# Kernel tuning notes

Hardware: AMD Instinct MI355X
Metric: run time of the kernel (lower is better)

## Reference

```python
import jax, jax.numpy as jnp
import numpy as np

EPS = 1e-5

def _fake_quant(w, axis):
    # symmetric int8 fake-quant with straight-through estimator
    s = jnp.max(jnp.abs(w), axis=axis, keepdims=True) / 127.0 + 1e-8
    q = jnp.clip(jnp.round(w / s), -127.0, 127.0) * s
    return w + jax.lax.stop_gradient(q - w)

def _qconv1x1(x, w, b):
    # x: [B, C_in, Q, H, W]; w: [C_out, C_in] (1x1 kernel); weight fake-quantized
    wq = _fake_quant(w, axis=1)
    return jnp.einsum('bcqhw,oc->boqhw', x, wq) + b[None, :, None, None, None]

def setup_inputs() -> dict:
    key = jax.random.key(0)
    ks = jax.random.split(key, 12)
    B, C, Q, H, W = 8, 256, 4, 40, 40
    x = jax.random.normal(ks[0], (B, C, Q, H, W), dtype=jnp.float32)
    scale = 1.0 / np.sqrt(C)
    Wq = jax.random.normal(ks[1], (C, C), dtype=jnp.float32) * scale
    Wk = jax.random.normal(ks[2], (C, C), dtype=jnp.float32) * scale
    Wv = jax.random.normal(ks[3], (C, C), dtype=jnp.float32) * scale
    Wp = jax.random.normal(ks[4], (C, C), dtype=jnp.float32) * scale
    bq = jnp.zeros((C,), jnp.float32)
    bk = jnp.zeros((C,), jnp.float32)
    bv = jnp.zeros((C,), jnp.float32)
    bp = jnp.zeros((C,), jnp.float32)
    gamma = jnp.ones((C,), jnp.float32)
    beta = jnp.zeros((C,), jnp.float32)
    return {"x": x, "Wq": Wq, "bq": bq, "Wk": Wk, "bk": bk,
            "Wv": Wv, "bv": bv, "Wp": Wp, "bp": bp,
            "gamma": gamma, "beta": beta}

def reference(x, Wq, bq, Wk, bk, Wv, bv, Wp, bp, gamma, beta):
    B, C, Q, H, W = x.shape
    q = _qconv1x1(x, Wq, bq)
    k = _qconv1x1(x, Wk, bk)
    v = _qconv1x1(x, Wv, bv)
    # per-rotation channel attention: [B, Q=4, C, H*W]
    qh = q.reshape(B, C, Q, H * W).transpose(0, 2, 1, 3)
    kh = k.reshape(B, C, Q, H * W).transpose(0, 2, 1, 3)
    vh = v.reshape(B, C, Q, H * W).transpose(0, 2, 1, 3)
    scale = 1.0 / jnp.sqrt(jnp.float32(C // 4))
    attn = jnp.einsum('bqcn,bqdn->bqcd', qh, kh) * scale  # [B,4,C,C]
    attn = jax.nn.softmax(attn, axis=-1)
    out = jnp.einsum('bqcd,bqdn->bqcn', attn, vh)  # [B,4,C,HW]
    out = out.transpose(0, 2, 1, 3).reshape(B, C, Q, H, W)
    out = _qconv1x1(out, Wp, bp)
    # IQBN: per-channel batchnorm with int8 fake-quantized gamma
    mean = jnp.mean(out, axis=(0, 2, 3, 4), keepdims=True)
    var = jnp.var(out, axis=(0, 2, 3, 4), keepdims=True)
    g = _fake_quant(gamma, axis=None)[None, :, None, None, None]
    b = beta[None, :, None, None, None]
    out = (out - mean) * jax.lax.rsqrt(var + EPS) * g + b
    return out
```

## Files before the change

kernel.cpp:

```cpp
#include <hip/hip_runtime.h>
#include <math.h>

#define BB 8
#define CCH 256
#define QQ 4
#define NN 1600
#define BQN 32
#define SP 51200
#define EPSF 1e-5f

typedef __attribute__((ext_vector_type(8))) short bf16x8;
typedef __attribute__((ext_vector_type(4))) float f32x4;

static __device__ inline ushort f2bf(float f) {
  union { float f; unsigned u; } v; v.f = f;
  return (ushort)((v.u + 0x7fffu + ((v.u >> 16) & 1u)) >> 16);
}
static __device__ inline float bf2f(ushort u) {
  union { unsigned u; float f; } v; v.u = ((unsigned)u) << 16;
  return v.f;
}
static __device__ inline void gld16(const ushort* g, ushort* l) {
  __builtin_amdgcn_global_load_lds(
      (const __attribute__((address_space(1))) unsigned int*)g,
      (__attribute__((address_space(3))) unsigned int*)l, 16, 0, 0);
}

__global__ __launch_bounds__(256)
void qp_kernel(const float* __restrict__ Wq, const float* __restrict__ Wk,
               const float* __restrict__ Wv, const float* __restrict__ Wp,
               const float* __restrict__ gamma, const float* __restrict__ x,
               ushort* __restrict__ wq, ushort* __restrict__ wk,
               ushort* __restrict__ wvT, ushort* __restrict__ wp,
               ushort* __restrict__ wqT, ushort* __restrict__ wkT,
               ushort* __restrict__ wpT, float* __restrict__ gq,
               ushort* __restrict__ xb, ushort* __restrict__ xT,
               float* __restrict__ rpart) {
  __shared__ float red[256];
  __shared__ ushort lT[64 * 66];
  int blk = blockIdx.x;
  int tid = threadIdx.x;
  if (blk < 1024) {
    int mat = blk >> 8;
    int row = blk & 255;
    const float* W = (mat == 0) ? Wq : (mat == 1) ? Wk : (mat == 2) ? Wv : Wp;
    float w = W[row * 256 + tid];
    red[tid] = fabsf(w);
    __syncthreads();
    for (int s = 128; s > 0; s >>= 1) {
      if (tid < s) red[tid] = fmaxf(red[tid], red[tid + s]);
      __syncthreads();
    }
    float s = red[0] / 127.0f + 1e-8f;
    float q = fminf(fmaxf(rintf(w / s), -127.0f), 127.0f) * s;
    ushort qb = f2bf(q);
    if (mat == 0)      { wq[row * 256 + tid] = qb; wqT[tid * 256 + row] = qb; }
    else if (mat == 1) { wk[row * 256 + tid] = qb; wkT[tid * 256 + row] = qb; }
    else if (mat == 2) { wvT[tid * 256 + row] = qb; }
    else               { wp[row * 256 + tid] = qb; wpT[tid * 256 + row] = qb; }
    return;
  }
  if (blk == 1024) {
    float g = gamma[tid];
    red[tid] = fabsf(g);
    __syncthreads();
    for (int s = 128; s > 0; s >>= 1) {
      if (tid < s) red[tid] = fmaxf(red[tid], red[tid + s]);
      __syncthreads();
    }
    float s = red[0] / 127.0f + 1e-8f;
    gq[tid] = fminf(fmaxf(rintf(g / s), -127.0f), 127.0f) * s;
    return;
  }
  int p = blk - 1025;
  int sx = p % 25;
  int rem = p / 25;
  int cy = rem & 3, bqi = rem >> 2;
  int b = bqi >> 2, q = bqi & 3;
  int s0 = sx * 64, c0 = cy * 64;
  int c = tid >> 2, nch = (tid & 3) * 16;
  const float* xp = x + ((size_t)(b * CCH + c0 + c) * QQ + q) * NN + s0 + nch;
  union { ushort u[16]; int4 v[2]; } nb;
  float s = 0.f;
#pragma unroll
  for (int j = 0; j < 4; j++) {
    float4 f = ((const float4*)xp)[j];
    ushort b0 = f2bf(f.x), b1 = f2bf(f.y), b2 = f2bf(f.z), b3 = f2bf(f.w);
    s += bf2f(b0) + bf2f(b1) + bf2f(b2) + bf2f(b3);
    nb.u[j * 4 + 0] = b0;
    nb.u[j * 4 + 1] = b1;
    nb.u[j * 4 + 2] = b2;
    nb.u[j * 4 + 3] = b3;
    lT[c * 66 + nch + j * 4 + 0] = b0;
    lT[c * 66 + nch + j * 4 + 1] = b1;
    lT[c * 66 + nch + j * 4 + 2] = b2;
    lT[c * 66 + nch + j * 4 + 3] = b3;
  }
  ushort* xbp = xb + (size_t)bqi * (CCH * NN) + (size_t)(c0 + c) * NN + s0 + nch;
  *(int4*)xbp = nb.v[0];
  *((int4*)xbp + 1) = nb.v[1];
  s += __shfl_down(s, 2);
  s += __shfl_down(s, 1);
  if ((tid & 3) == 0) rpart[((size_t)bqi * 25 + sx) * 256 + c0 + c] = s;
  __syncthreads();
  int n = tid >> 2, cch = (tid & 3) * 16;
  union { ushort u[16]; int4 v[2]; } o;
#pragma unroll
  for (int i = 0; i < 16; i++) o.u[i] = lT[(cch + i) * 66 + n];
  ushort* dst = xT + (size_t)(bqi * NN + s0 + n) * CCH + c0 + cch;
  *(int4*)dst = o.v[0];
  *((int4*)dst + 1) = o.v[1];
}

__global__ __launch_bounds__(256)
void gram_uv_kernel(const ushort* __restrict__ xb, ushort* __restrict__ Gh,
                    ushort* __restrict__ Gl,
                    const ushort* __restrict__ wqT, const ushort* __restrict__ wkT,
                    const float* __restrict__ rpart, float* __restrict__ r,
                    float* __restrict__ u, float* __restrict__ vv) {
  __shared__ __align__(16) char smem[16384];
  __shared__ float rs[256];
  int t = blockIdx.x, z = blockIdx.y;
  int tid = threadIdx.x;
  if (t == 10) {
    float rv = 0.f;
#pragma unroll
    for (int k = 0; k < 25; k++) rv += rpart[((size_t)z * 25 + k) * 256 + tid];
    rs[tid] = rv;
    r[z * 256 + tid] = rv;
    __syncthreads();
    float su = 0.f, sv = 0.f;
    for (int i = 0; i < 256; i++) {
      float rr = rs[i];
      su += bf2f(wqT[i * 256 + tid]) * rr;
      sv += bf2f(wkT[i * 256 + tid]) * rr;
    }
    u[z * 256 + tid] = su;
    vv[z * 256 + tid] = sv;
    return;
  }
  int ty = (t >= 4) + (t >= 7) + (t >= 9);
  int base = ty * 4 - (ty * (ty - 1)) / 2;
  int tx = ty + (t - base);
  int mBase = ty * 64, nBase = tx * 64;
  bool offd = (tx != ty);
  int wave = tid >> 6, lane = tid & 63;
  int wm = wave >> 1, wn = wave & 1;
  int col = lane & 15, quad = lane >> 4;
  const ushort* X = xb + (size_t)z * (CCH * NN);
  const ushort* gA = X + (size_t)(mBase + (tid >> 2)) * NN + (tid & 3) * 8;
  const ushort* gB = X + (size_t)(nBase + (tid >> 2)) * NN + (tid & 3) * 8;
  f32x4 acc[2][2];
#pragma unroll
  for (int i = 0; i < 2; i++)
#pragma unroll
    for (int j = 0; j < 2; j++) acc[i][j] = (f32x4){0.f, 0.f, 0.f, 0.f};

  const int nIter = NN / 32;
  gld16(gA, (ushort*)smem + tid * 8);
  gld16(gB, (ushort*)(smem + 4096) + tid * 8);
  for (int it = 0; it < nIter; ++it) {
    int cur = it & 1;
    __syncthreads();
    if (it + 1 < nIter) {
      int kt = (it + 1) << 5;
      char* bb = smem + (cur ^ 1) * 8192;
      gld16(gA + kt, (ushort*)bb + tid * 8);
      gld16(gB + kt, (ushort*)(bb + 4096) + tid * 8);
    }
    const ushort* lA = (const ushort*)(smem + cur * 8192);
    const ushort* lB = lA + 2048;
    bf16x8 af[2], bfr[2];
#pragma unroll
    for (int i = 0; i < 2; i++)
      af[i] = *(const bf16x8*)&lA[(wm * 32 + i * 16 + col) * 32 + quad * 8];
#pragma unroll
    for (int j = 0; j < 2; j++)
      bfr[j] = *(const bf16x8*)&lB[(wn * 32 + j * 16 + col) * 32 + quad * 8];
#pragma unroll
    for (int i = 0; i < 2; i++)
#pragma unroll
      for (int j = 0; j < 2; j++)
        acc[i][j] = __builtin_amdgcn_mfma_f32_16x16x32_bf16(af[i], bfr[j], acc[i][j], 0, 0, 0);
  }
  __syncthreads();
  float* lCw = (float*)smem + wave * 576;
#pragma unroll
  for (int i = 0; i < 2; i++) {
#pragma unroll
    for (int j = 0; j < 2; j++)
#pragma unroll
      for (int rg = 0; rg < 4; rg++)
        lCw[(quad * 4 + rg) * 36 + j * 16 + col] = acc[i][j][rg];
    int mrow0 = mBase + wm * 32 + i * 16;
    int nW = nBase + wn * 32;
    int rr = lane >> 2, cc = (lane & 3) * 8;
    union { ushort u[8]; int4 v; } oh, ol;
#pragma unroll
    for (int t8 = 0; t8 < 8; t8++) {
      float vfl = lCw[rr * 36 + cc + t8];
      ushort hh = f2bf(vfl);
      oh.u[t8] = hh;
      ol.u[t8] = f2bf(vfl - bf2f(hh));
    }
    size_t off = (size_t)z * 65536 + (size_t)(mrow0 + rr) * 256 + nW + cc;
    *(int4*)(Gh + off) = oh.v;
    *(int4*)(Gl + off) = ol.v;
    if (offd) {
      int nn = lane >> 1, mh = (lane & 1) * 8;
      union { ushort u[8]; int4 v; } th, tl;
#pragma unroll
      for (int t8 = 0; t8 < 8; t8++) {
        float vfl = lCw[(mh + t8) * 36 + nn];
        ushort hh = f2bf(vfl);
        th.u[t8] = hh;
        tl.u[t8] = f2bf(vfl - bf2f(hh));
      }
      size_t offT = (size_t)z * 65536 + (size_t)(nW + nn) * 256 + mrow0 + mh;
      *(int4*)(Gh + offT) = th.v;
      *(int4*)(Gl + offT) = tl.v;
    }
  }
}

__global__ __launch_bounds__(256)
void spk_kernel(const ushort* __restrict__ wq, const ushort* __restrict__ Gh,
                const ushort* __restrict__ Gl, const ushort* __restrict__ wk,
                const float* __restrict__ ug, const float* __restrict__ vg,
                const float* __restrict__ bqv, const float* __restrict__ bkv,
                const float* __restrict__ bvv,
                ushort* __restrict__ P, float* __restrict__ pb) {
  __shared__ __align__(16) char smem[103424];
  int z = blockIdx.y, mBase = blockIdx.x * 32;
  int tid = threadIdx.x, wave = tid >> 6, lane = tid & 63;
  int col = lane & 15, quad = lane >> 4;
  int rA = tid >> 2, sub = (tid & 3) * 8;
  const ushort* Ghz = Gh + (size_t)z * 65536;
  const ushort* Glz = Gl + (size_t)z * 65536;
  ushort* M1h_l = (ushort*)(smem + 69632);
  ushort* M1l_l = M1h_l + 8448;

  f32x4 acc[2][4];
#pragma unroll
  for (int i = 0; i < 2; i++)
#pragma unroll
    for (int j = 0; j < 4; j++) acc[i][j] = (f32x4){0.f, 0.f, 0.f, 0.f};

  auto s1_load = [&](int buf, int kt) {
    ushort* L = (ushort*)(smem + buf * 34816);
    if (tid < 128)
      gld16(wq + (size_t)(mBase + rA) * 256 + kt + sub, L + tid * 8);
    ushort* Lh = L + 1024;
    ushort* Ll = L + 9216;
#pragma unroll
    for (int q = 0; q < 4; q++) {
      int n = q * 64 + rA;
      gld16(Ghz + (size_t)n * 256 + kt + sub, Lh + (q * 256 + tid) * 8);
      gld16(Glz + (size_t)n * 256 + kt + sub, Ll + (q * 256 + tid) * 8);
    }
  };
  s1_load(0, 0);
  for (int it = 0; it < 8; ++it) {
    int cur = it & 1;
    __syncthreads();
    if (it + 1 < 8) s1_load(cur ^ 1, (it + 1) * 32);
    const ushort* L = (const ushort*)(smem + cur * 34816);
    const ushort* lA = L;
    const ushort* lBh = L + 1024;
    const ushort* lBl = L + 9216;
    bf16x8 af[2], bh[4], bl[4];
#pragma unroll
    for (int i = 0; i < 2; i++)
      af[i] = *(const bf16x8*)&lA[(i * 16 + col) * 32 + quad * 8];
#pragma unroll
    for (int j = 0; j < 4; j++) {
      bh[j] = *(const bf16x8*)&lBh[(wave * 64 + j * 16 + col) * 32 + quad * 8];
      bl[j] = *(const bf16x8*)&lBl[(wave * 64 + j * 16 + col) * 32 + quad * 8];
    }
#pragma unroll
    for (int i = 0; i < 2; i++)
#pragma unroll
      for (int j = 0; j < 4; j++) {
        acc[i][j] = __builtin_amdgcn_mfma_f32_16x16x32_bf16(af[i], bh[j], acc[i][j], 0, 0, 0);
        acc[i][j] = __builtin_amdgcn_mfma_f32_16x16x32_bf16(af[i], bl[j], acc[i][j], 0, 0, 0);
      }
  }
#pragma unroll
  for (int i = 0; i < 2; i++)
#pragma unroll
    for (int j = 0; j < 4; j++)
#pragma unroll
      for (int rg = 0; rg < 4; rg++) {
        int ml = i * 16 + quad * 4 + rg;
        int cg = wave * 64 + j * 16 + col;
        float vfl = acc[i][j][rg];
        ushort hh = f2bf(vfl);
        M1h_l[ml * 264 + cg] = hh;
        M1l_l[ml * 264 + cg] = f2bf(vfl - bf2f(hh));
      }

  f32x4 acc2[2][4];
#pragma unroll
  for (int i = 0; i < 2; i++)
#pragma unroll
    for (int j = 0; j < 4; j++) acc2[i][j] = (f32x4){0.f, 0.f, 0.f, 0.f};
  auto s2_load = [&](int buf, int kt) {
    ushort* L = (ushort*)(smem + buf * 34816);
#pragma unroll
    for (int q = 0; q < 4; q++)
      gld16(wk + (size_t)(q * 64 + rA) * 256 + kt + sub, L + (q * 256 + tid) * 8);
  };
  s2_load(0, 0);
  for (int it = 0; it < 8; ++it) {
    int cur = it & 1;
    __syncthreads();
    if (it + 1 < 8) s2_load(cur ^ 1, (it + 1) * 32);
    const ushort* lB = (const ushort*)(smem + cur * 34816);
    int kt = it * 32;
    bf16x8 ah[2], al[2], bfr[4];
#pragma unroll
    for (int i = 0; i < 2; i++) {
      ah[i] = *(const bf16x8*)&M1h_l[(i * 16 + col) * 264 + kt + quad * 8];
      al[i] = *(const bf16x8*)&M1l_l[(i * 16 + col) * 264 + kt + quad * 8];
    }
#pragma unroll
    for (int j = 0; j < 4; j++)
      bfr[j] = *(const bf16x8*)&lB[(wave * 64 + j * 16 + col) * 32 + quad * 8];
#pragma unroll
    for (int i = 0; i < 2; i++)
#pragma unroll
      for (int j = 0; j < 4; j++) {
        acc2[i][j] = __builtin_amdgcn_mfma_f32_16x16x32_bf16(ah[i], bfr[j], acc2[i][j], 0, 0, 0);
        acc2[i][j] = __builtin_amdgcn_mfma_f32_16x16x32_bf16(al[i], bfr[j], acc2[i][j], 0, 0, 0);
      }
  }
  __syncthreads();

  float* Sb = (float*)(smem + 69632);
  float bkc[4], vvc[4];
#pragma unroll
  for (int j = 0; j < 4; j++) {
    int cg = wave * 64 + j * 16 + col;
    bkc[j] = bkv[cg];
    vvc[j] = vg[z * 256 + cg];
  }
#pragma unroll
  for (int i = 0; i < 2; i++)
#pragma unroll
    for (int rg = 0; rg < 4; rg++) {
      int ml = i * 16 + quad * 4 + rg;
      int rglob = mBase + ml;
      float uu = ug[z * 256 + rglob];
      float bqc = bqv[rglob];
#pragma unroll
      for (int j = 0; j < 4; j++)
        Sb[ml * 260 + wave * 64 + j * 16 + col] =
            0.125f * (acc2[i][j][rg] + uu * bkc[j] + bqc * vvc[j] + 1600.0f * bqc * bkc[j]);
    }
  __syncthreads();

  float4 bv4 = *(const float4*)(bvv + lane * 4);
#pragma unroll
  for (int rr8 = 0; rr8 < 8; ++rr8) {
    int rloc = wave * 8 + rr8;
    f32x4 sv = *(const f32x4*)&Sb[rloc * 260 + lane * 4];
    float x0 = sv[0], x1 = sv[1], x2 = sv[2], x3 = sv[3];
    float m = fmaxf(fmaxf(x0, x1), fmaxf(x2, x3));
#pragma unroll
    for (int s = 32; s > 0; s >>= 1) m = fmaxf(m, __shfl_xor(m, s));
    float e0 = expf(x0 - m), e1 = expf(x1 - m), e2 = expf(x2 - m), e3 = expf(x3 - m);
    float t = e0 + e1 + e2 + e3;
#pragma unroll
    for (int s = 32; s > 0; s >>= 1) t += __shfl_xor(t, s);
    float is = 1.0f / t;
    float p0 = e0 * is, p1 = e1 * is, p2 = e2 * is, p3 = e3 * is;
    union { ushort u[4]; uint2 v; } o;
    o.u[0] = f2bf(p0); o.u[1] = f2bf(p1); o.u[2] = f2bf(p2); o.u[3] = f2bf(p3);
    *(uint2*)(P + (size_t)z * 65536 + (size_t)(mBase + rloc) * 256 + lane * 4) = o.v;
    float d = p0 * bv4.x + p1 * bv4.y + p2 * bv4.z + p3 * bv4.w;
#pragma unroll
    for (int s = 32; s > 0; s >>= 1) d += __shfl_xor(d, s);
    if (lane == 0) pb[z * 256 + mBase + rloc] = d;
  }
}

__global__ __launch_bounds__(256)
void pt_kernel(const ushort* __restrict__ P, const ushort* __restrict__ wvT,
               const ushort* __restrict__ wp,
               ushort* __restrict__ Tm, ushort* __restrict__ TmT,
               float* __restrict__ m_acc, float* __restrict__ v_acc) {
  __shared__ __align__(16) char smem[53760];
  int z = blockIdx.y, cs = blockIdx.x * 32;
  int tid = threadIdx.x, wave = tid >> 6, lane = tid & 63;
  int col = lane & 15, quad = lane >> 4;
  int rA = tid >> 2, sub = (tid & 3) * 8;
  if (blockIdx.x == 0 && blockIdx.y == 0) {
    m_acc[tid] = 0.f;
    v_acc[tid] = 0.f;
  }
  const ushort* Pz = P + (size_t)z * 65536;
  ushort* N1b = (ushort*)(smem + 36864);

  f32x4 acc[4][2];
#pragma unroll
  for (int i = 0; i < 4; i++)
#pragma unroll
    for (int j = 0; j < 2; j++) acc[i][j] = (f32x4){0.f, 0.f, 0.f, 0.f};
  auto s3_load = [&](int buf, int kt) {
    ushort* L = (ushort*)(smem + buf * 18432);
#pragma unroll
    for (int q = 0; q < 4; q++)
      gld16(Pz + (size_t)(q * 64 + rA) * 256 + kt + sub, L + (q * 256 + tid) * 8);
    if (tid < 128)
      gld16(wvT + (size_t)(cs + rA) * 256 + kt + sub, L + 8192 + tid * 8);
  };
  s3_load(0, 0);
  for (int it = 0; it < 8; ++it) {
    int cur = it & 1;
    __syncthreads();
    if (it + 1 < 8) s3_load(cur ^ 1, (it + 1) * 32);
    const ushort* lP = (const ushort*)(smem + cur * 18432);
    const ushort* lV = lP + 8192;
    bf16x8 af[4], bfr[2];
#pragma unroll
    for (int i = 0; i < 4; i++)
      af[i] = *(const bf16x8*)&lP[(wave * 64 + i * 16 + col) * 32 + quad * 8];
#pragma unroll
    for (int j = 0; j < 2; j++)
      bfr[j] = *(const bf16x8*)&lV[(j * 16 + col) * 32 + quad * 8];
#pragma unroll
    for (int i = 0; i < 4; i++)
#pragma unroll
      for (int j = 0; j < 2; j++)
        acc[i][j] = __builtin_amdgcn_mfma_f32_16x16x32_bf16(af[i], bfr[j], acc[i][j], 0, 0, 0);
  }
#pragma unroll
  for (int i = 0; i < 4; i++)
#pragma unroll
    for (int j = 0; j < 2; j++)
#pragma unroll
      for (int rg = 0; rg < 4; rg++) {
        int e = wave * 64 + i * 16 + quad * 4 + rg;
        int cl = j * 16 + col;
        N1b[cl * 264 + e] = f2bf(acc[i][j][rg]);
      }

  f32x4 acc2[4][2];
#pragma unroll
  for (int i = 0; i < 4; i++)
#pragma unroll
    for (int j = 0; j < 2; j++) acc2[i][j] = (f32x4){0.f, 0.f, 0.f, 0.f};
  auto s4_load = [&](int buf, int kt) {
    ushort* L = (ushort*)(smem + buf * 18432);
#pragma unroll
    for (int q = 0; q < 4; q++)
      gld16(wp + (size_t)(q * 64 + rA) * 256 + kt + sub, L + (q * 256 + tid) * 8);
  };
  s4_load(0, 0);
  for (int it = 0; it < 8; ++it) {
    int cur = it & 1;
    __syncthreads();
    if (it + 1 < 8) s4_load(cur ^ 1, (it + 1) * 32);
    const ushort* lW = (const ushort*)(smem + cur * 18432);
    int kt = it * 32;
    bf16x8 af[4], bfr[2];
#pragma unroll
    for (int i = 0; i < 4; i++)
      af[i] = *(const bf16x8*)&lW[(wave * 64 + i * 16 + col) * 32 + quad * 8];
#pragma unroll
    for (int j = 0; j < 2; j++)
      bfr[j] = *(const bf16x8*)&N1b[(j * 16 + col) * 264 + kt + quad * 8];
#pragma unroll
    for (int i = 0; i < 4; i++)
#pragma unroll
      for (int j = 0; j < 2; j++)
        acc2[i][j] = __builtin_amdgcn_mfma_f32_16x16x32_bf16(af[i], bfr[j], acc2[i][j], 0, 0, 0);
  }
  __syncthreads();
  float* lCw = (float*)smem + wave * 576;
#pragma unroll
  for (int i = 0; i < 4; i++) {
#pragma unroll
    for (int j = 0; j < 2; j++)
#pragma unroll
      for (int rg = 0; rg < 4; rg++)
        lCw[(quad * 4 + rg) * 36 + j * 16 + col] = acc2[i][j][rg];
    int oW = wave * 64 + i * 16;
    int rr = lane >> 2, cc = (lane & 3) * 8;
    union { ushort u[8]; int4 v; } o;
#pragma unroll
    for (int t8 = 0; t8 < 8; t8++) o.u[t8] = f2bf(lCw[rr * 36 + cc + t8]);
    *(int4*)(Tm + (size_t)z * 65536 + (size_t)(oW + rr) * 256 + cs + cc) = o.v;
    int nn = lane >> 1, mh = (lane & 1) * 8;
    union { ushort u[8]; int4 v; } o2;
#pragma unroll
    for (int t8 = 0; t8 < 8; t8++) o2.u[t8] = f2bf(lCw[(mh + t8) * 36 + nn]);
    *(int4*)(TmT + (size_t)z * 65536 + (size_t)(cs + nn) * 256 + oW + mh) = o2.v;
  }
}

__global__ __launch_bounds__(256)
void dsq_bo_kernel(const ushort* __restrict__ Tm, const ushort* __restrict__ Gh,
                   const ushort* __restrict__ Gl,
                   const ushort* __restrict__ wpT, const ushort* __restrict__ TmT,
                   const float* __restrict__ pb, const float* __restrict__ rb,
                   const float* __restrict__ bp, float* __restrict__ bo,
                   float* __restrict__ m_acc, float* __restrict__ v_acc) {
  __shared__ __align__(16) char smem[24576];
  int blk = blockIdx.x;
  int tid = threadIdx.x;
  if (blk >= 512) {
    int z = blk - 512;
    float* sp = (float*)smem;
    float* sr = sp + 256;
    sp[tid] = pb[z * 256 + tid];
    sr[tid] = rb[z * 256 + tid];
    __syncthreads();
    float bv = bp[tid], d1 = 0.f;
    const ushort* Tz = TmT + (size_t)z * 65536;
    for (int c = 0; c < 256; c++) {
      bv += bf2f(wpT[c * 256 + tid]) * sp[c];
      d1 += bf2f(Tz[c * 256 + tid]) * sr[c];
    }
    bo[z * 256 + tid] = bv;
    atomicAdd(m_acc + tid, d1 + 1600.0f * bv);
    atomicAdd(v_acc + tid, 2.0f * bv * d1 + 1600.0f * bv * bv);
    return;
  }
  int z = blk >> 4;
  int mBase = ((blk >> 2) & 3) * 64, nBase = (blk & 3) * 64;
  int wave = tid >> 6, lane = tid & 63;
  int wm = wave >> 1, wn = wave & 1;
  int col = lane & 15, quad = lane >> 4;
  int srow = tid >> 2, skc = (tid & 3) * 8;
  const ushort* Tz = Tm + (size_t)z * 65536;
  const ushort* gA = Tz + (size_t)(mBase + srow) * 256 + skc;
  const ushort* gB = Gh + (size_t)z * 65536 + (size_t)(nBase + srow) * 256 + skc;
  const ushort* gX = Gl + (size_t)z * 65536 + (size_t)(nBase + srow) * 256 + skc;

  f32x4 acc[2][2];
#pragma unroll
  for (int i = 0; i < 2; i++)
#pragma unroll
    for (int j = 0; j < 2; j++) acc[i][j] = (f32x4){0.f, 0.f, 0.f, 0.f};

  {
    char* bb = smem;
    gld16(gA, (ushort*)bb + tid * 8);
    gld16(gB, (ushort*)(bb + 4096) + tid * 8);
    gld16(gX, (ushort*)(bb + 8192) + tid * 8);
  }
  for (int it = 0; it < 8; ++it) {
    int cur = it & 1;
    __syncthreads();
    if (it + 1 < 8) {
      int kt = (it + 1) * 32;
      char* bb = smem + (cur ^ 1) * 12288;
      gld16(gA + kt, (ushort*)bb + tid * 8);
      gld16(gB + kt, (ushort*)(bb + 4096) + tid * 8);
      gld16(gX + kt, (ushort*)(bb + 8192) + tid * 8);
    }
    const ushort* lA = (const ushort*)(smem + cur * 12288);
    const ushort* lB = lA + 2048;
    const ushort* lX = lA + 4096;
    bf16x8 af[2], bfv[2], xf[2];
#pragma unroll
    for (int i = 0; i < 2; i++)
      af[i] = *(const bf16x8*)&lA[(wm * 32 + i * 16 + col) * 32 + quad * 8];
#pragma unroll
    for (int j = 0; j < 2; j++) {
      bfv[j] = *(const bf16x8*)&lB[(wn * 32 + j * 16 + col) * 32 + quad * 8];
      xf[j]  = *(const bf16x8*)&lX[(wn * 32 + j * 16 + col) * 32 + quad * 8];
    }
#pragma unroll
    for (int i = 0; i < 2; i++)
#pragma unroll
      for (int j = 0; j < 2; j++) {
        acc[i][j] = __builtin_amdgcn_mfma_f32_16x16x32_bf16(af[i], bfv[j], acc[i][j], 0, 0, 0);
        acc[i][j] = __builtin_amdgcn_mfma_f32_16x16x32_bf16(af[i], xf[j], acc[i][j], 0, 0, 0);
      }
  }
#pragma unroll
  for (int i = 0; i < 2; i++) {
    int mr = mBase + wm * 32 + i * 16 + quad * 4;
#pragma unroll
    for (int rg = 0; rg < 4; rg++) {
      float p = 0.f;
#pragma unroll
      for (int j = 0; j < 2; j++)
        p += acc[i][j][rg] * bf2f(Tz[(mr + rg) * 256 + nBase + wn * 32 + j * 16 + col]);
      p += __shfl_down(p, 8);
      p += __shfl_down(p, 4);
      p += __shfl_down(p, 2);
      p += __shfl_down(p, 1);
      if (col == 0) atomicAdd(v_acc + mr + rg, p);
    }
  }
}

__global__ __launch_bounds__(256)
void final_kernel(const ushort* __restrict__ Tm, const ushort* __restrict__ xT,
                  const float* __restrict__ bo, const float* __restrict__ m_acc,
                  const float* __restrict__ v_acc, const float* __restrict__ gq,
                  const float* __restrict__ beta, float* __restrict__ out) {
  __shared__ __align__(16) char smem[32768];
  float* lC = (float*)smem;
  int z = blockIdx.z;
  int mBase = blockIdx.y * 128, nBase = blockIdx.x * 128;
  int tid = threadIdx.x, wave = tid >> 6, lane = tid & 63;
  int wm = wave >> 1, wn = wave & 1;
  int col = lane & 15, quad = lane >> 4;
  int srow = tid >> 2, skc = (tid & 3) * 8;
  const ushort* Az = Tm + (size_t)z * 65536;
  const ushort* Bz = xT + (size_t)z * (NN * 256);
  const ushort* gA  = Az + (size_t)(mBase + srow) * 256 + skc;
  const ushort* gA2 = gA + 64 * 256;
  int br1 = nBase + srow;      br1 = br1 < NN ? br1 : NN - 1;
  int br2 = nBase + 64 + srow; br2 = br2 < NN ? br2 : NN - 1;
  const ushort* gB  = Bz + (size_t)br1 * 256 + skc;
  const ushort* gB2 = Bz + (size_t)br2 * 256 + skc;
  ushort* sA1[2]; ushort* sA2[2]; ushort* sB1[2]; ushort* sB2[2];
#pragma unroll
  for (int b = 0; b < 2; b++) {
    ushort* lAb = (ushort*)(smem + b * 16384);
    ushort* lBb = (ushort*)(smem + b * 16384 + 8192);
    sA1[b] = &lAb[srow * 32 + skc];
    sA2[b] = &lAb[(64 + srow) * 32 + skc];
    sB1[b] = &lBb[srow * 32 + skc];
    sB2[b] = &lBb[(64 + srow) * 32 + skc];
  }
  f32x4 acc[4][4];
#pragma unroll
  for (int i = 0; i < 4; i++)
#pragma unroll
    for (int j = 0; j < 4; j++) acc[i][j] = (f32x4){0.f, 0.f, 0.f, 0.f};

  const int nIter = 8;
  gld16(gA, sA1[0]); gld16(gA2, sA2[0]); gld16(gB, sB1[0]); gld16(gB2, sB2[0]);
  for (int it = 0; it < nIter; ++it) {
    int cur = it & 1;
    __syncthreads();
    if (it + 1 < nIter) {
      int kt = (it + 1) << 5, nxt = cur ^ 1;
      gld16(gA + kt, sA1[nxt]); gld16(gA2 + kt, sA2[nxt]);
      gld16(gB + kt, sB1[nxt]); gld16(gB2 + kt, sB2[nxt]);
    }
    const ushort* lAc = (const ushort*)(smem + cur * 16384);
    const ushort* lBc = (const ushort*)(smem + cur * 16384 + 8192);
    bf16x8 af[4], bfr[4];
#pragma unroll
    for (int i = 0; i < 4; i++)
      af[i] = *(const bf16x8*)&lAc[(wm * 64 + i * 16 + col) * 32 + quad * 8];
#pragma unroll
    for (int j = 0; j < 4; j++)
      bfr[j] = *(const bf16x8*)&lBc[(wn * 64 + j * 16 + col) * 32 + quad * 8];
#pragma unroll
    for (int i = 0; i < 4; i++)
#pragma unroll
      for (int j = 0; j < 4; j++)
        acc[i][j] = __builtin_amdgcn_mfma_f32_16x16x32_bf16(af[i], bfr[j], acc[i][j], 0, 0, 0);
  }
  __syncthreads();
  float* lCw = lC + wave * 16 * 68;
  int mW = mBase + wm * 64, nW = nBase + wn * 64;
  int b = z >> 2, q = z & 3;
  const float inv = 1.0f / (float)SP;
#pragma unroll
  for (int i = 0; i < 4; i++) {
#pragma unroll
    for (int j = 0; j < 4; j++)
#pragma unroll
      for (int rg = 0; rg < 4; rg++)
        lCw[(quad * 4 + rg) * 68 + j * 16 + col] = acc[i][j][rg];
    int mrow0 = mW + i * 16;
    int rr = lane & 15, cc = lane >> 4;
    int n0 = nW + cc * 16;
    int o = mrow0 + rr;
    float bi = bo[(size_t)z * 256 + o];
    float mean = m_acc[o] * inv;
    float var = v_acc[o] * inv - mean * mean;
    float scl = rsqrtf(var + EPSF) * gq[o];
    float be = beta[o];
    if (n0 < NN) {
      float* C = out + (size_t)b * (CCH * QQ * NN)
               + (size_t)o * (QQ * NN) + (size_t)q * NN + n0;
#pragma unroll
      for (int v = 0; v < 4; v++) {
        float4 f;
        f.x = (lCw[rr * 68 + cc * 16 + v * 4 + 0] + bi - mean) * scl + be;
        f.y = (lCw[rr * 68 + cc * 16 + v * 4 + 1] + bi - mean) * scl + be;
        f.z = (lCw[rr * 68 + cc * 16 + v * 4 + 2] + bi - mean) * scl + be;
        f.w = (lCw[rr * 68 + cc * 16 + v * 4 + 3] + bi - mean) * scl + be;
        *(float4*)(C + v * 4) = f;
      }
    }
  }
}

extern "C" void kernel_launch(void* const* d_in, const int* in_sizes, int n_in,
                              void* d_out, int out_size, void* d_ws, size_t ws_size,
                              hipStream_t stream) {
  const float* x     = (const float*)d_in[0];
  const float* Wq    = (const float*)d_in[1];
  const float* bq    = (const float*)d_in[2];
  const float* Wk    = (const float*)d_in[3];
  const float* bk    = (const float*)d_in[4];
  const float* Wv    = (const float*)d_in[5];
  const float* bv    = (const float*)d_in[6];
  const float* Wp    = (const float*)d_in[7];
  const float* bp    = (const float*)d_in[8];
  const float* gamma = (const float*)d_in[9];
  const float* beta  = (const float*)d_in[10];
  float* out = (float*)d_out;

  ushort* h    = (ushort*)d_ws;
  ushort* wq   = h;
  ushort* wk   = wq + 65536;
  ushort* wp   = wk + 65536;
  ushort* wvT  = wp + 65536;
  ushort* wqT  = wvT + 65536;
  ushort* wkT  = wqT + 65536;
  ushort* wpT  = wkT + 65536;
  ushort* xb   = wpT + 65536;
  ushort* xT   = xb + (size_t)BQN * CCH * NN;
  ushort* Gh   = xT + (size_t)BQN * CCH * NN;
  ushort* Gl   = Gh + (size_t)BQN * 65536;
  ushort* P    = Gl + (size_t)BQN * 65536;
  ushort* Tm   = P + (size_t)BQN * 65536;
  ushort* TmT  = Tm + (size_t)BQN * 65536;
  float*  r    = (float*)(TmT + (size_t)BQN * 65536);
  float*  u    = r + 8192;
  float*  vv   = u + 8192;
  float*  pb   = vv + 8192;
  float*  bo   = pb + 8192;
  float*  m_acc = bo + 8192;
  float*  v_acc = m_acc + 256;
  float*  gq   = v_acc + 256;
  float*  rpart = gq + 256;

  qp_kernel<<<4225, 256, 0, stream>>>(Wq, Wk, Wv, Wp, gamma, x,
                                      wq, wk, wvT, wp, wqT, wkT, wpT, gq,
                                      xb, xT, rpart);
  gram_uv_kernel<<<dim3(11, BQN), 256, 0, stream>>>(xb, Gh, Gl, wqT, wkT,
                                                    rpart, r, u, vv);
  spk_kernel<<<dim3(8, BQN), 256, 0, stream>>>(wq, Gh, Gl, wk, u, vv, bq, bk, bv, P, pb);
  pt_kernel<<<dim3(8, BQN), 256, 0, stream>>>(P, wvT, wp, Tm, TmT, m_acc, v_acc);
  dsq_bo_kernel<<<544, 256, 0, stream>>>(Tm, Gh, Gl, wpT, TmT, pb, r, bp,
                                         bo, m_acc, v_acc);
  final_kernel<<<dim3(13, 2, BQN), 256, 0, stream>>>(Tm, xT, bo, m_acc, v_acc,
                                                     gq, beta, out);
}
```

Baseline: 254.6 us.

## Halve row tiles in spk/pt kernels and read operands directly from global memory

The spk and pt kernels now handle 16-row/column tiles instead of 32, which doubles the grid to 512 blocks. They also drop the LDS double-buffered global_load_lds staging and load MFMA operands straight from global memory (L2-cached) into registers. A block-index swizzle spreads consecutive blocks across batch slices. Shared memory per block shrinks sharply, which should raise occupancy and spread the work over more CUs. The cost is redundant global/L2 traffic, since each weight tile is reread by more blocks with no LDS reuse, and the loads are no longer overlapped through explicit prefetch.

```diff
diff --git a/kernel.cpp b/kernel.cpp
--- a/kernel.cpp
+++ b/kernel.cpp
@@ -19,6 +19,9 @@
 static __device__ inline float bf2f(ushort u) {
   union { unsigned u; float f; } v; v.u = ((unsigned)u) << 16;
   return v.f;
+}
+static __device__ inline bf16x8 ldg8(const ushort* p) {
+  return *(const bf16x8*)p;
 }
 static __device__ inline void gld16(const ushort* g, ushort* l) {
   __builtin_amdgcn_global_load_lds(
@@ -230,139 +233,91 @@
                 const float* __restrict__ bqv, const float* __restrict__ bkv,
                 const float* __restrict__ bvv,
                 ushort* __restrict__ P, float* __restrict__ pb) {
-  __shared__ __align__(16) char smem[103424];
-  int z = blockIdx.y, mBase = blockIdx.x * 32;
-  int tid = threadIdx.x, wave = tid >> 6, lane = tid & 63;
+  __shared__ __align__(16) char smem[16896];
+  ushort* M1h_l = (ushort*)smem;
+  ushort* M1l_l = M1h_l + 4224;
+  int lin = blockIdx.x + 16 * blockIdx.y;
+  int nl = (lin & 7) * 64 + (lin >> 3);
+  int mBase = (nl & 15) * 16, z = nl >> 4;
+  int tid = threadIdx.x, w = tid >> 6, lane = tid & 63;
   int col = lane & 15, quad = lane >> 4;
-  int rA = tid >> 2, sub = (tid & 3) * 8;
   const ushort* Ghz = Gh + (size_t)z * 65536;
   const ushort* Glz = Gl + (size_t)z * 65536;
-  ushort* M1h_l = (ushort*)(smem + 69632);
-  ushort* M1l_l = M1h_l + 8448;
-
-  f32x4 acc[2][4];
-#pragma unroll
-  for (int i = 0; i < 2; i++)
-#pragma unroll
-    for (int j = 0; j < 4; j++) acc[i][j] = (f32x4){0.f, 0.f, 0.f, 0.f};
-
-  auto s1_load = [&](int buf, int kt) {
-    ushort* L = (ushort*)(smem + buf * 34816);
-    if (tid < 128)
-      gld16(wq + (size_t)(mBase + rA) * 256 + kt + sub, L + tid * 8);
-    ushort* Lh = L + 1024;
-    ushort* Ll = L + 9216;
-#pragma unroll
-    for (int q = 0; q < 4; q++) {
-      int n = q * 64 + rA;
-      gld16(Ghz + (size_t)n * 256 + kt + sub, Lh + (q * 256 + tid) * 8);
-      gld16(Glz + (size_t)n * 256 + kt + sub, Ll + (q * 256 + tid) * 8);
-    }
-  };
-  s1_load(0, 0);
-  for (int it = 0; it < 8; ++it) {
-    int cur = it & 1;
-    __syncthreads();
-    if (it + 1 < 8) s1_load(cur ^ 1, (it + 1) * 32);
-    const ushort* L = (const ushort*)(smem + cur * 34816);
-    const ushort* lA = L;
-    const ushort* lBh = L + 1024;
-    const ushort* lBl = L + 9216;
-    bf16x8 af[2], bh[4], bl[4];
-#pragma unroll
-    for (int i = 0; i < 2; i++)
-      af[i] = *(const bf16x8*)&lA[(i * 16 + col) * 32 + quad * 8];
+
+  f32x4 acc[4];
+#pragma unroll
+  for (int j = 0; j < 4; j++) acc[j] = (f32x4){0.f, 0.f, 0.f, 0.f};
+  bf16x8 af[8];
+  {
+    const ushort* pA = wq + (size_t)(mBase + col) * 256 + quad * 8;
+#pragma unroll
+    for (int kk = 0; kk < 8; kk++) af[kk] = ldg8(pA + kk * 32);
+  }
+#pragma unroll
+  for (int kk = 0; kk < 8; kk++) {
 #pragma unroll
     for (int j = 0; j < 4; j++) {
-      bh[j] = *(const bf16x8*)&lBh[(wave * 64 + j * 16 + col) * 32 + quad * 8];
-      bl[j] = *(const bf16x8*)&lBl[(wave * 64 + j * 16 + col) * 32 + quad * 8];
-    }
-#pragma unroll
-    for (int i = 0; i < 2; i++)
-#pragma unroll
-      for (int j = 0; j < 4; j++) {
-        acc[i][j] = __builtin_amdgcn_mfma_f32_16x16x32_bf16(af[i], bh[j], acc[i][j], 0, 0, 0);
-        acc[i][j] = __builtin_amdgcn_mfma_f32_16x16x32_bf16(af[i], bl[j], acc[i][j], 0, 0, 0);
-      }
-  }
-#pragma unroll
-  for (int i = 0; i < 2; i++)
-#pragma unroll
-    for (int j = 0; j < 4; j++)
-#pragma unroll
-      for (int rg = 0; rg < 4; rg++) {
-        int ml = i * 16 + quad * 4 + rg;
-        int cg = wave * 64 + j * 16 + col;
-        float vfl = acc[i][j][rg];
-        ushort hh = f2bf(vfl);
-        M1h_l[ml * 264 + cg] = hh;
-        M1l_l[ml * 264 + cg] = f2bf(vfl - bf2f(hh));
-      }
-
-  f32x4 acc2[2][4];
-#pragma unroll
-  for (int i = 0; i < 2; i++)
-#pragma unroll
-    for (int j = 0; j < 4; j++) acc2[i][j] = (f32x4){0.f, 0.f, 0.f, 0.f};
-  auto s2_load = [&](int buf, int kt) {
-    ushort* L = (ushort*)(smem + buf * 34816);
-#pragma unroll
-    for (int q = 0; q < 4; q++)
-      gld16(wk + (size_t)(q * 64 + rA) * 256 + kt + sub, L + (q * 256 + tid) * 8);
-  };
-  s2_load(0, 0);
-  for (int it = 0; it < 8; ++it) {
-    int cur = it & 1;
-    __syncthreads();
-    if (it + 1 < 8) s2_load(cur ^ 1, (it + 1) * 32);
-    const ushort* lB = (const ushort*)(smem + cur * 34816);
-    int kt = it * 32;
-    bf16x8 ah[2], al[2], bfr[4];
-#pragma unroll
-    for (int i = 0; i < 2; i++) {
-      ah[i] = *(const bf16x8*)&M1h_l[(i * 16 + col) * 264 + kt + quad * 8];
-      al[i] = *(const bf16x8*)&M1l_l[(i * 16 + col) * 264 + kt + quad * 8];
-    }
-#pragma unroll
-    for (int j = 0; j < 4; j++)
-      bfr[j] = *(const bf16x8*)&lB[(wave * 64 + j * 16 + col) * 32 + quad * 8];
-#pragma unroll
-    for (int i = 0; i < 2; i++)
-#pragma unroll
-      for (int j = 0; j < 4; j++) {
-        acc2[i][j] = __builtin_amdgcn_mfma_f32_16x16x32_bf16(ah[i], bfr[j], acc2[i][j], 0, 0, 0);
-        acc2[i][j] = __builtin_amdgcn_mfma_f32_16x16x32_bf16(al[i], bfr[j], acc2[i][j], 0, 0, 0);
-      }
-  }
+      size_t ro = (size_t)(w * 64 + j * 16 + col) * 256 + kk * 32 + quad * 8;
+      bf16x8 bh = ldg8(Ghz + ro);
+      bf16x8 bl = ldg8(Glz + ro);
+      acc[j] = __builtin_amdgcn_mfma_f32_16x16x32_bf16(af[kk], bh, acc[j], 0, 0, 0);
+      acc[j] = __builtin_amdgcn_mfma_f32_16x16x32_bf16(af[kk], bl, acc[j], 0, 0, 0);
+    }
+  }
+#pragma unroll
+  for (int j = 0; j < 4; j++)
+#pragma unroll
+    for (int rg = 0; rg < 4; rg++) {
+      int ml = quad * 4 + rg;
+      int cg = w * 64 + j * 16 + col;
+      float vfl = acc[j][rg];
+      ushort hh = f2bf(vfl);
+      M1h_l[ml * 264 + cg] = hh;
+      M1l_l[ml * 264 + cg] = f2bf(vfl - bf2f(hh));
+    }
   __syncthreads();
 
-  float* Sb = (float*)(smem + 69632);
+  f32x4 acc2[4];
+#pragma unroll
+  for (int j = 0; j < 4; j++) acc2[j] = (f32x4){0.f, 0.f, 0.f, 0.f};
+#pragma unroll
+  for (int kk = 0; kk < 8; kk++) {
+    bf16x8 ah = *(const bf16x8*)&M1h_l[col * 264 + kk * 32 + quad * 8];
+    bf16x8 al = *(const bf16x8*)&M1l_l[col * 264 + kk * 32 + quad * 8];
+#pragma unroll
+    for (int j = 0; j < 4; j++) {
+      bf16x8 b = ldg8(wk + (size_t)(w * 64 + j * 16 + col) * 256 + kk * 32 + quad * 8);
+      acc2[j] = __builtin_amdgcn_mfma_f32_16x16x32_bf16(ah, b, acc2[j], 0, 0, 0);
+      acc2[j] = __builtin_amdgcn_mfma_f32_16x16x32_bf16(al, b, acc2[j], 0, 0, 0);
+    }
+  }
+  __syncthreads();
+
+  float* Sb = (float*)smem;
   float bkc[4], vvc[4];
 #pragma unroll
   for (int j = 0; j < 4; j++) {
-    int cg = wave * 64 + j * 16 + col;
+    int cg = w * 64 + j * 16 + col;
     bkc[j] = bkv[cg];
     vvc[j] = vg[z * 256 + cg];
   }
 #pragma unroll
-  for (int i = 0; i < 2; i++)
-#pragma unroll
-    for (int rg = 0; rg < 4; rg++) {
-      int ml = i * 16 + quad * 4 + rg;
-      int rglob = mBase + ml;
-      float uu = ug[z * 256 + rglob];
-      float bqc = bqv[rglob];
-#pragma unroll
-      for (int j = 0; j < 4; j++)
-        Sb[ml * 260 + wave * 64 + j * 16 + col] =
-            0.125f * (acc2[i][j][rg] + uu * bkc[j] + bqc * vvc[j] + 1600.0f * bqc * bkc[j]);
-    }
+  for (int rg = 0; rg < 4; rg++) {
+    int ml = quad * 4 + rg;
+    int rglob = mBase + ml;
+    float uu = ug[z * 256 + rglob];
+    float bqc = bqv[rglob];
+#pragma unroll
+    for (int j = 0; j < 4; j++)
+      Sb[ml * 260 + w * 64 + j * 16 + col] =
+          0.125f * (acc2[j][rg] + uu * bkc[j] + bqc * vvc[j] + 1600.0f * bqc * bkc[j]);
+  }
   __syncthreads();
 
   float4 bv4 = *(const float4*)(bvv + lane * 4);
 #pragma unroll
-  for (int rr8 = 0; rr8 < 8; ++rr8) {
-    int rloc = wave * 8 + rr8;
+  for (int rr4 = 0; rr4 < 4; ++rr4) {
+    int rloc = w * 4 + rr4;
     f32x4 sv = *(const f32x4*)&Sb[rloc * 260 + lane * 4];
     float x0 = sv[0], x1 = sv[1], x2 = sv[2], x3 = sv[3];
     float m = fmaxf(fmaxf(x0, x1), fmaxf(x2, x3));
@@ -389,113 +344,78 @@
                const ushort* __restrict__ wp,
                ushort* __restrict__ Tm, ushort* __restrict__ TmT,
                float* __restrict__ m_acc, float* __restrict__ v_acc) {
-  __shared__ __align__(16) char smem[53760];
-  int z = blockIdx.y, cs = blockIdx.x * 32;
-  int tid = threadIdx.x, wave = tid >> 6, lane = tid & 63;
+  __shared__ __align__(16) char smem[17664];
+  ushort* N1b = (ushort*)smem;
+  float* lCwB = (float*)(smem + 8448);
+  int lin = blockIdx.x + 16 * blockIdx.y;
+  int nl = (lin & 7) * 64 + (lin >> 3);
+  int cs = (nl & 15) * 16, z = nl >> 4;
+  int tid = threadIdx.x, w = tid >> 6, lane = tid & 63;
   int col = lane & 15, quad = lane >> 4;
-  int rA = tid >> 2, sub = (tid & 3) * 8;
-  if (blockIdx.x == 0 && blockIdx.y == 0) {
+  if (nl == 0) {
     m_acc[tid] = 0.f;
     v_acc[tid] = 0.f;
   }
   const ushort* Pz = P + (size_t)z * 65536;
-  ushort* N1b = (ushort*)(smem + 36864);
-
-  f32x4 acc[4][2];
+
+  f32x4 acc[4];
+#pragma unroll
+  for (int i = 0; i < 4; i++) acc[i] = (f32x4){0.f, 0.f, 0.f, 0.f};
+  bf16x8 bv8[8];
+  {
+    const ushort* pV = wvT + (size_t)(cs + col) * 256 + quad * 8;
+#pragma unroll
+    for (int kk = 0; kk < 8; kk++) bv8[kk] = ldg8(pV + kk * 32);
+  }
+#pragma unroll
+  for (int kk = 0; kk < 8; kk++) {
+#pragma unroll
+    for (int i = 0; i < 4; i++) {
+      bf16x8 a = ldg8(Pz + (size_t)(w * 64 + i * 16 + col) * 256 + kk * 32 + quad * 8);
+      acc[i] = __builtin_amdgcn_mfma_f32_16x16x32_bf16(a, bv8[kk], acc[i], 0, 0, 0);
+    }
+  }
 #pragma unroll
   for (int i = 0; i < 4; i++)
 #pragma unroll
-    for (int j = 0; j < 2; j++) acc[i][j] = (f32x4){0.f, 0.f, 0.f, 0.f};
-  auto s3_load = [&](int buf, int kt) {
-    ushort* L = (ushort*)(smem + buf * 18432);
-#pragma unroll
-    for (int q = 0; q < 4; q++)
-      gld16(Pz + (size_t)(q * 64 + rA) * 256 + kt + sub, L + (q * 256 + tid) * 8);
-    if (tid < 128)
-      gld16(wvT + (size_t)(cs + rA) * 256 + kt + sub, L + 8192 + tid * 8);
-  };
-  s3_load(0, 0);
-  for (int it = 0; it < 8; ++it) {
-    int cur = it & 1;
-    __syncthreads();
-    if (it + 1 < 8) s3_load(cur ^ 1, (it + 1) * 32);
-    const ushort* lP = (const ushort*)(smem + cur * 18432);
-    const ushort* lV = lP + 8192;
-    bf16x8 af[4], bfr[2];
-#pragma unroll
-    for (int i = 0; i < 4; i++)
-      af[i] = *(const bf16x8*)&lP[(wave * 64 + i * 16 + col) * 32 + quad * 8];
-#pragma unroll
-    for (int j = 0; j < 2; j++)
-      bfr[j] = *(const bf16x8*)&lV[(j * 16 + col) * 32 + quad * 8];
-#pragma unroll
-    for (int i = 0; i < 4; i++)
-#pragma unroll
-      for (int j = 0; j < 2; j++)
-        acc[i][j] = __builtin_amdgcn_mfma_f32_16x16x32_bf16(af[i], bfr[j], acc[i][j], 0, 0, 0);
-  }
-#pragma unroll
-  for (int i = 0; i < 4; i++)
-#pragma unroll
-    for (int j = 0; j < 2; j++)
-#pragma unroll
-      for (int rg = 0; rg < 4; rg++) {
-        int e = wave * 64 + i * 16 + quad * 4 + rg;
-        int cl = j * 16 + col;
-        N1b[cl * 264 + e] = f2bf(acc[i][j][rg]);
-      }
-
-  f32x4 acc2[4][2];
-#pragma unroll
-  for (int i = 0; i < 4; i++)
-#pragma unroll
-    for (int j = 0; j < 2; j++) acc2[i][j] = (f32x4){0.f, 0.f, 0.f, 0.f};
-  auto s4_load = [&](int buf, int kt) {
-    ushort* L = (ushort*)(smem + buf * 18432);
-#pragma unroll
-    for (int q = 0; q < 4; q++)
-      gld16(wp + (size_t)(q * 64 + rA) * 256 + kt + sub, L + (q * 256 + tid) * 8);
-  };
-  s4_load(0, 0);
-  for (int it = 0; it < 8; ++it) {
-    int cur = it & 1;
-    __syncthreads();
-    if (it + 1 < 8) s4_load(cur ^ 1, (it + 1) * 32);
-    const ushort* lW = (const ushort*)(smem + cur * 18432);
-    int kt = it * 32;
-    bf16x8 af[4], bfr[2];
-#pragma unroll
-    for (int i = 0; i < 4; i++)
-      af[i] = *(const bf16x8*)&lW[(wave * 64 + i * 16 + col) * 32 + quad * 8];
-#pragma unroll
-    for (int j = 0; j < 2; j++)
-      bfr[j] = *(const bf16x8*)&N1b[(j * 16 + col) * 264 + kt + quad * 8];
-#pragma unroll
-    for (int i = 0; i < 4; i++)
-#pragma unroll
-      for (int j = 0; j < 2; j++)
-        acc2[i][j] = __builtin_amdgcn_mfma_f32_16x16x32_bf16(af[i], bfr[j], acc2[i][j], 0, 0, 0);
-  }
+    for (int rg = 0; rg < 4; rg++) {
+      int e = w * 64 + i * 16 + quad * 4 + rg;
+      N1b[col * 264 + e] = f2bf(acc[i][rg]);
+    }
   __syncthreads();
-  float* lCw = (float*)smem + wave * 576;
+
+  f32x4 acc2[4];
+#pragma unroll
+  for (int i = 0; i < 4; i++) acc2[i] = (f32x4){0.f, 0.f, 0.f, 0.f};
+  bf16x8 bn[8];
+#pragma unroll
+  for (int kk = 0; kk < 8; kk++)
+    bn[kk] = *(const bf16x8*)&N1b[col * 264 + kk * 32 + quad * 8];
+#pragma unroll
+  for (int kk = 0; kk < 8; kk++) {
+#pragma unroll
+    for (int i = 0; i < 4; i++) {
+      bf16x8 a = ldg8(wp + (size_t)(w * 64 + i * 16 + col) * 256 + kk * 32 + quad * 8);
+      acc2[i] = __builtin_amdgcn_mfma_f32_16x16x32_bf16(a, bn[kk], acc2[i], 0, 0, 0);
+    }
+  }
+  float* lCw = lCwB + w * 576;
 #pragma unroll
   for (int i = 0; i < 4; i++) {
 #pragma unroll
-    for (int j = 0; j < 2; j++)
-#pragma unroll
-      for (int rg = 0; rg < 4; rg++)
-        lCw[(quad * 4 + rg) * 36 + j * 16 + col] = acc2[i][j][rg];
-    int oW = wave * 64 + i * 16;
-    int rr = lane >> 2, cc = (lane & 3) * 8;
-    union { ushort u[8]; int4 v; } o;
-#pragma unroll
-    for (int t8 = 0; t8 < 8; t8++) o.u[t8] = f2bf(lCw[rr * 36 + cc + t8]);
-    *(int4*)(Tm + (size_t)z * 65536 + (size_t)(oW + rr) * 256 + cs + cc) = o.v;
-    int nn = lane >> 1, mh = (lane & 1) * 8;
-    union { ushort u[8]; int4 v; } o2;
-#pragma unroll
-    for (int t8 = 0; t8 < 8; t8++) o2.u[t8] = f2bf(lCw[(mh + t8) * 36 + nn]);
-    *(int4*)(TmT + (size_t)z * 65536 + (size_t)(cs + nn) * 256 + oW + mh) = o2.v;
+    for (int rg = 0; rg < 4; rg++)
+      lCw[(quad * 4 + rg) * 36 + col] = acc2[i][rg];
+    int oW = w * 64 + i * 16;
+    int rr = lane & 15, cc4 = (lane >> 4) * 4;
+    union { ushort u[4]; uint2 v; } o;
+#pragma unroll
+    for (int t8 = 0; t8 < 4; t8++) o.u[t8] = f2bf(lCw[rr * 36 + cc4 + t8]);
+    *(uint2*)(Tm + (size_t)z * 65536 + (size_t)(oW + rr) * 256 + cs + cc4) = o.v;
+    int nn = lane & 15, mh = (lane >> 4) * 4;
+    union { ushort u[4]; uint2 v; } o2;
+#pragma unroll
+    for (int t8 = 0; t8 < 4; t8++) o2.u[t8] = f2bf(lCw[(mh + t8) * 36 + nn]);
+    *(uint2*)(TmT + (size_t)z * 65536 + (size_t)(cs + nn) * 256 + oW + mh) = o2.v;
   }
 }
 
@@ -743,8 +663,8 @@
                                       xb, xT, rpart);
   gram_uv_kernel<<<dim3(11, BQN), 256, 0, stream>>>(xb, Gh, Gl, wqT, wkT,
                                                     rpart, r, u, vv);
-  spk_kernel<<<dim3(8, BQN), 256, 0, stream>>>(wq, Gh, Gl, wk, u, vv, bq, bk, bv, P, pb);
-  pt_kernel<<<dim3(8, BQN), 256, 0, stream>>>(P, wvT, wp, Tm, TmT, m_acc, v_acc);
+  spk_kernel<<<dim3(16, BQN), 256, 0, stream>>>(wq, Gh, Gl, wk, u, vv, bq, bk, bv, P, pb);
+  pt_kernel<<<dim3(16, BQN), 256, 0, stream>>>(P, wvT, wp, Tm, TmT, m_acc, v_acc);
   dsq_bo_kernel<<<544, 256, 0, stream>>>(Tm, Gh, Gl, wpT, TmT, pb, r, bp,
                                          bo, m_acc, v_acc);
   final_kernel<<<dim3(13, 2, BQN), 256, 0, stream>>>(Tm, xT, bo, m_acc, v_acc,
```

Result: slower. 267.2 us (+5.0%).
